# Optimization experiments

Hardware: AMD Instinct MI355X
Metric: run time of the kernel (lower is better)

## Reference

```python
import jax, jax.numpy as jnp
import numpy as np

_SAMPLING_EPS = 1e-5
_NEG_INF = -jnp.inf


def _apply_min_p(logits, min_p):
    # probs >= min_p * max_prob are kept (vLLM apply_min_p)
    probs = jax.nn.softmax(logits, axis=-1)
    max_p = jnp.max(probs, axis=-1, keepdims=True)
    keep = probs >= (min_p[:, None] * max_p)
    return jnp.where(keep, logits, _NEG_INF)


def _apply_top_k_top_p(logits, top_k, top_p):
    # One descending sort serves both filters (mirrors vLLM topk/topp kernel).
    T, V = logits.shape
    sorted_l = jnp.sort(logits, axis=-1)[:, ::-1]  # [T, V] descending
    # top-k threshold: k-th largest logit; top_k <= 0 means disabled
    k = jnp.where(top_k <= 0, V, jnp.clip(top_k, 1, V)).astype(jnp.int32)
    kth = jnp.take_along_axis(sorted_l, (k - 1)[:, None], axis=-1)  # [T, 1]
    # top-p: keep smallest prefix whose prob mass reaches top_p (first token always kept)
    probs = jax.nn.softmax(sorted_l, axis=-1)
    cum = jnp.cumsum(probs, axis=-1)
    keep_p = (cum - probs) < top_p[:, None]
    pth = jnp.min(jnp.where(keep_p, sorted_l, jnp.inf), axis=-1, keepdims=True)
    keep = (logits >= kth) & (logits >= pth)
    return jnp.where(keep, logits, _NEG_INF)


def _gather_logprobs(logprobs, num_logprobs, token_ids):
    # vLLM gather_logprobs: topk + sampled-token logprob + rank
    topk_lp, topk_idx = jax.lax.top_k(logprobs, num_logprobs)  # [T, K]
    tok = token_ids[:, None]  # [T, 1]
    tok_lp = jnp.take_along_axis(logprobs, tok, axis=-1)  # [T, 1]
    ranks = jnp.sum(logprobs >= tok_lp, axis=-1).astype(jnp.int32)  # [T]
    indices = jnp.concatenate([tok, topk_idx], axis=1).astype(jnp.int32)
    lps = jnp.concatenate([tok_lp, topk_lp], axis=1)
    return indices, lps, ranks


def setup_inputs() -> dict:
    key = jax.random.key(0)
    k1, k2, k3, k4, k5, k6 = jax.random.split(key, 6)
    T, V = 256, 128256
    logits = jax.random.normal(k1, (T, V), dtype=jnp.float32)
    temperature = 0.2 + 1.3 * jax.random.uniform(k2, (T,), dtype=jnp.float32)
    # every 8th request is greedy (temperature < _SAMPLING_EPS path)
    temperature = jnp.where(jnp.arange(T) % 8 == 0, 0.0, temperature)
    min_p = 0.05 * jax.random.uniform(k3, (T,), dtype=jnp.float32)
    top_p = 0.5 + 0.5 * jax.random.uniform(k4, (T,), dtype=jnp.float32)
    top_k = jax.random.randint(k5, (T,), 0, 64, dtype=jnp.int32)
    u = jax.random.uniform(k6, (T, V), dtype=jnp.float32, minval=1e-10, maxval=1.0)
    return {"logits": logits, "temperature": temperature, "min_p": min_p,
            "top_p": top_p, "top_k": top_k, "u": u, "num_logprobs": 20}


def reference(logits, temperature, min_p, top_p, top_k, u, num_logprobs):
    logits = logits.astype(jnp.float32)
    # logprobs computed on raw (pre-temperature) logits, as in vLLM
    raw_logprobs = jax.nn.log_softmax(logits, axis=-1)
    # greedy path
    greedy = jnp.argmax(logits, axis=-1)
    # random path: temperature -> min_p -> top-k/top-p -> gumbel-max sample
    is_greedy = temperature < _SAMPLING_EPS
    safe_temp = jnp.where(is_greedy, 1.0, temperature)  # rows with temp<eps use greedy anyway
    l = logits / safe_temp[:, None]
    l = _apply_min_p(l, min_p)
    l = _apply_top_k_top_p(l, top_k, top_p)
    gumbel = -jnp.log(-jnp.log(u))  # u in (0,1)
    random_sampled = jnp.argmax(l + gumbel, axis=-1)
    sampled = jnp.where(is_greedy, greedy, random_sampled)
    indices, lps, ranks = _gather_logprobs(raw_logprobs, num_logprobs, sampled)
    sampled_token_ids = sampled.astype(jnp.int32)[:, None]  # [T, 1]
    return sampled_token_ids, indices, lps, ranks
```

## Files before the change

kernel.cpp:

```cpp
#include <hip/hip_runtime.h>
#include <math.h>

#define TPB 1024
#define TPBS 256
#define NS 8
#define NBINS 512
#define CAP 2048
#define NSEL 64
#define MBINS 1024
#define MWIN 16.0f
#define WIN 2.0f
#define SLCAP 1024
#define BANDCAP 64

typedef unsigned long long u64t;

__device__ __forceinline__ unsigned int ordAsc(float v) {
  unsigned int b = __float_as_uint(v);
  return (b & 0x80000000u) ? ~b : (b | 0x80000000u);
}
__device__ __forceinline__ float ordInv(unsigned int o) {
  return __uint_as_float((o & 0x80000000u) ? (o & 0x7fffffffu) : ~o);
}
__device__ __forceinline__ unsigned int fkeyDesc(float v) { return ~ordAsc(v); }
// ... 41 lines not shown
  __syncthreads();
  return r;
}
__device__ __forceinline__ u64t blockMaxU64(u64t v, u64t* sred) {
  #pragma unroll
  for (int o = 32; o > 0; o >>= 1) { u64t v2 = __shfl_down(v, o, 64); if (v2 > v) v = v2; }
  int wid = threadIdx.x >> 6, lane = threadIdx.x & 63, nw = blockDim.x >> 6;
  __syncthreads();
  if (lane == 0) sred[wid] = v;
  __syncthreads();
  if (threadIdx.x == 0) { u64t r = sred[0]; for (int w = 1; w < nw; ++w) if (sred[w] > r) r = sred[w]; sred[0] = r; }
  __syncthreads();
  u64t r = sred[0];
  __syncthreads();
  return r;
}
__device__ __forceinline__ void blockArgMaxF(float& v, int& idx, float* sredf, int* sredi) {
  #pragma unroll
  for (int o = 32; o > 0; o >>= 1) {
    float v2 = __shfl_down(v, o, 64);
    int  i2 = __shfl_down(idx, o, 64);
    if (v2 > v || (v2 == v && i2 < idx)) { v = v2; idx = i2; }
  }
  int wid = threadIdx.x >> 6, lane = threadIdx.x & 63, nw = blockDim.x >> 6;
  __syncthreads();
  if (lane == 0) { sredf[wid] = v; sredi[wid] = idx; }
  __syncthreads();
  if (threadIdx.x == 0) {
    float bv = sredf[0]; int bi = sredi[0];
    for (int w = 1; w < nw; ++w) {
      float v2 = sredf[w]; int i2 = sredi[w];
      if (v2 > bv || (v2 == bv && i2 < bi)) { bv = v2; bi = i2; }
    }
    sredf[0] = bv; sredi[0] = bi;
  }
  __syncthreads();
  v = sredf[0]; idx = sredi[0];
  __syncthreads();
}

__device__ void bitonicSortN(u64t* keys, int n) {
  for (unsigned int k = 2; k <= (unsigned int)n; k <<= 1) {
    for (unsigned int j = k >> 1; j > 0; j >>= 1) {
      __syncthreads();
      for (unsigned int i = threadIdx.x; i < (unsigned int)n; i += blockDim.x) {
        unsigned int ixj = i ^ j;
        if (ixj > i) {
          u64t a = keys[i], b = keys[ixj];
          bool up = ((i & k) == 0);
          if ((a > b) == up) { keys[i] = b; keys[ixj] = a; }
        }
      }
    }
  }
  __syncthreads();
}

__device__ u64t bitonicReg1024(u64t key, u64t* lds) {
  const int tid = threadIdx.x;
  for (unsigned int k = 2; k <= 1024; k <<= 1) {
    for (unsigned int j = k >> 1; j > 0; j >>= 1) {
      u64t partner;
      if (j >= 64) {
        __syncthreads();
        lds[tid] = key;
        __syncthreads();
        partner = lds[tid ^ j];
      } else {
        partner = __shfl_xor((unsigned long long)key, (int)j, 64);
      }
      bool up = ((tid & k) == 0);
      bool lower = ((tid & j) == 0);
      bool keepSmaller = (up == lower);
      bool pSmaller = (partner < key);
      if (keepSmaller == pSmaller) key = partner;
    }
  }
  __syncthreads();
  lds[tid] = key;
  __syncthreads();
  return key;
}

__global__ __launch_bounds__(TPBS) void k1_max(const float* __restrict__ logits,
                                               u64t* __restrict__ maxes,
                                               int* __restrict__ ccnt,
                                               int* __restrict__ bandcnt,
                                               u64t* __restrict__ mass, int V) {
  const int row = blockIdx.y, s = blockIdx.x, tid = threadIdx.x;
  {
    const int per = MBINS / NS;
    u64t* m = mass + (size_t)row * MBINS + s * per;
    for (int b = tid; b < per; b += TPBS) m[b] = 0ull;
    if (s == 0 && tid == 0) { ccnt[row] = 0; bandcnt[row] = 0; }
  }
  const float* x = logits + (size_t)row * V;
  const int V4 = V >> 2;
  const float4* x4 = (const float4*)x;
  const int a4 = (int)(((long long)V4 * s) / NS), b4 = (int)(((long long)V4 * (s + 1)) / NS);
  u64t best = 0ull;
  for (int i4 = a4 + tid; i4 < b4; i4 += TPBS) {
    float4 v = x4[i4]; int b = i4 << 2;
    u64t k0 = mkMaxKey(v.x, b);     if (k0 > best) best = k0;
    u64t k1 = mkMaxKey(v.y, b + 1); if (k1 > best) best = k1;
    u64t k2 = mkMaxKey(v.z, b + 2); if (k2 > best) best = k2;
    u64t k3 = mkMaxKey(v.w, b + 3); if (k3 > best) best = k3;
  }
  if (s == NS - 1) for (int i = (V4 << 2) + tid; i < V; i += TPBS) {
    u64t k = mkMaxKey(x[i], i); if (k > best) best = k;
  }
  __shared__ u64t sred[16];
  best = blockMaxU64(best, sred);
  if (tid == 0) maxes[row * NS + s] = best;
}

__global__ __launch_bounds__(TPBS) void k2_all(const float* __restrict__ logits,
    const float* __restrict__ temp_arr, const float* __restrict__ minp_arr,
    const int* __restrict__ topk_arr, const u64t* __restrict__ maxes,
    float* __restrict__ s0_ws, float* __restrict__ sl_ws,
    float* __restrict__ sp_ws, int* __restrict__ ck_ws,
    int* __restrict__ ccnt, u64t* __restrict__ cand,
    int* __restrict__ bandcnt, u64t* __restrict__ band,
    u64t* __restrict__ mass, int V) {
  const int row = blockIdx.y, s = blockIdx.x, tid = threadIdx.x;
  __shared__ u64t smax[NS];
  __shared__ float sredF[16];
  __shared__ int sredI[16];
  __shared__ u64t lcand[SLCAP];
  __shared__ u64t lmass[MBINS];
  __shared__ int lcnt, lbase;
  const float temp = temp_arr[row];
  const bool greedy = (temp < 1e-5f);
  const int topk = topk_arr[row];
  const bool deep = (!greedy && topk <= 0);
  if (tid < NS) smax[tid] = maxes[row * NS + tid];
  if (tid == 0) lcnt = 0;
  if (deep) for (int b = tid; b < MBINS; b += TPBS) lmass[b] = 0ull;
  __syncthreads();
  u64t mk = smax[0];
  for (int w = 1; w < NS; ++w) { u64t t = smax[w]; if (t > mk) mk = t; }
  const float m0 = ordInv((unsigned int)(mk >> 32));
  const float st = greedy ? 1.0f : temp;
  const float ml = m0 / st;
  const float wlo = m0 - WIN;
  const float minp = minp_arr[row];
  const float bHi = minp * (1.0f + 4e-6f);
  const float bLo = minp * (1.0f - 4e-6f);
  const float scaleM = (float)MBINS / MWIN;
  const float* x = logits + (size_t)row * V;
  const int V4 = V >> 2;
  const float4* x4 = (const float4*)x;
  const int a4 = (int)(((long long)V4 * s) / NS), b4 = (int)(((long long)V4 * (s + 1)) / NS);
  float s0 = 0.f, sl = 0.f, sp = 0.f; int ckp = 0;
  auto body = [&](float vv, int gi) {
    s0 += expf(vv - m0);
    if (!greedy) {
      float l = vv / st;
      float e = expf(l - ml);
      sl += e;
      if (minp <= 0.f || e > bHi) {
        sp += e; ckp++;
        if (deep) {
          float fm = (m0 - vv) * scaleM;
          if (fm < (float)MBINS)
            atomicAdd(&lmass[(int)fm], (u64t)((double)e * 4294967296.0));
        }
      } else if (e >= bLo) {
        int pos = atomicAdd(&bandcnt[row], 1);
        if (pos < BANDCAP)
          band[(size_t)row * BANDCAP + pos] = ((u64t)(unsigned int)gi << 32) | __float_as_uint(vv);
      }
    }
    if (vv >= wlo) {
      int pos = atomicAdd(&lcnt, 1);
      if (pos < SLCAP) lcand[pos] = ((u64t)fkeyDesc(vv) << 32) | (unsigned int)gi;
    }
  };
  for (int i4 = a4 + tid; i4 < b4; i4 += TPBS) {
    float4 v = x4[i4]; int b = i4 << 2;
    body(v.x, b); body(v.y, b + 1); body(v.z, b + 2); body(v.w, b + 3);
  }
  if (s == NS - 1) for (int i = (V4 << 2) + tid; i < V; i += TPBS) body(x[i], i);
  float r0 = blockSumF(s0, sredF);
  float rl = blockSumF(sl, sredF);
  float rp = blockSumF(sp, sredF);
  int rc = blockSumI(ckp, sredI);
  if (tid == 0) {
    s0_ws[row * NS + s] = r0; sl_ws[row * NS + s] = rl;
    sp_ws[row * NS + s] = rp; ck_ws[row * NS + s] = rc;
    int c = lcnt;
    int add = (c > SLCAP) ? (c + CAP + 1) : c;
    lbase = atomicAdd(&ccnt[row], add);
  }
  __syncthreads();
  int c = lcnt < SLCAP ? lcnt : SLCAP;
  int base = lbase;
  for (int j = tid; j < c; j += TPBS) {
    int pos = base + j;
    if (pos < CAP) cand[(size_t)row * CAP + pos] = lcand[j];
  }
  if (deep) {
    for (int b = tid; b < MBINS; b += TPBS) {
      u64t m = lmass[b];
      if (m) atomicAdd(&mass[(size_t)row * MBINS + b], m);
    }
  }
}

__global__ __launch_bounds__(TPB) void k5_final(const float* __restrict__ logits,
    const float* __restrict__ temp_arr, const float* __restrict__ minp_arr,
    const float* __restrict__ topp_arr, const int* __restrict__ topk_arr,
    const float* __restrict__ u_arr, const u64t* __restrict__ maxes,
    const float* __restrict__ s0_ws, const float* __restrict__ sl_ws,
    const float* __restrict__ sp_ws, const int* __restrict__ ck_ws,
    int* __restrict__ ccnt, const u64t* __restrict__ cand,
    const u64t* __restrict__ mass, const u64t* __restrict__ band,
    const int* __restrict__ bandcnt, float* __restrict__ w_thr,
    int* __restrict__ w_bpM, double* __restrict__ w_seed, float* __restrict__ w_spD,
    float* __restrict__ out, int T, int V, int NL) {
  __shared__ u64t keyA[CAP];
  __shared__ u64t keyB[CAP];
  __shared__ int fh[NBINS];
  __shared__ float sredF[16];
  __shared__ int sredI[16];
  __shared__ u64t smax[NS];
  __shared__ float sp0[NS], spl[NS], spsp[NS];
  __shared__ int spck[NS];
  __shared__ float sh_thresh, sh_toklp, sh_spAdd;
  __shared__ double sh_seed;
  __shared__ int sh_cnt, sh_bp, sh_bCnt, sh_ckAdd;
  __shared__ u64t sh_bKeys[BANDCAP];
  __shared__ u64t sh_bMass[BANDCAP];
  __shared__ int  sh_bBin[BANDCAP];

  const int row = blockIdx.x;
  const int tid = threadIdx.x;
  const float* x  = logits + (size_t)row * V;
  const float* uu = u_arr  + (size_t)row * V;
  const float temp = temp_arr[row];
  const float minp = minp_arr[row];
  const float topp = topp_arr[row];
  const int   topk = topk_arr[row];
  const bool greedy = (temp < 1e-5f);
  const float st = greedy ? 1.0f : temp;
  const int V4 = V >> 2;
  const float4* x4 = (const float4*)x;

  if (tid < NS) {
    smax[tid] = maxes[row * NS + tid];
    sp0[tid] = s0_ws[row * NS + tid];
    spl[tid] = sl_ws[row * NS + tid];
    spsp[tid] = sp_ws[row * NS + tid];
    spck[tid] = ck_ws[row * NS + tid];
  }
  __syncthreads();
  u64t mk = smax[0];
  for (int w = 1; w < NS; ++w) { u64t t = smax[w]; if (t > mk) mk = t; }
  const float m0 = ordInv((unsigned int)(mk >> 32));
  const int gidx = (int)(~(unsigned int)mk);
  float S0 = sp0[0], S = spl[0], Sp = spsp[0];
  int ck = spck[0];
  for (int w = 1; w < NS; ++w) { S0 += sp0[w]; S += spl[w]; Sp += spsp[w]; ck += spck[w]; }
  const float ml = m0 / st;
  const float logS0 = logf(S0);
  const float rhs = minp * (1.0f / S);
  const float rhsS = rhs * S;
  const float rhsHi = rhsS * (1.0f + 1e-6f);
  const float rhsLo = rhsS * (1.0f - 1e-6f);
  auto keepTest = [&](float e) -> bool {
    if (e > rhsHi) return true;
    if (e < rhsLo) return false;
    return (e / S) >= rhs;
  };
  const bool deep = (!greedy && topk <= 0);
  const float scaleM = (float)MBINS / MWIN;

  const int bandTotal = greedy ? 0 : bandcnt[row];
  const bool bandOv = bandTotal > BANDCAP;
  if (tid == 0) { sh_bCnt = 0; sh_spAdd = 0.f; sh_ckAdd = 0; }
  __syncthreads();
  if (!greedy && !bandOv && bandTotal > 0 && minp > 0.f) {
    if (tid == 0) {
      for (int i = 0; i < bandTotal; ++i) sh_bKeys[i] = band[(size_t)row * BANDCAP + i];
      for (int i = 1; i < bandTotal; ++i) {
        u64t k = sh_bKeys[i]; int j = i - 1;
        while (j >= 0 && sh_bKeys[j] > k) { sh_bKeys[j + 1] = sh_bKeys[j]; j--; }
        sh_bKeys[j + 1] = k;
      }
      float spAdd = 0.f; int ckAdd = 0, bc = 0;
      for (int i = 0; i < bandTotal; ++i) {
        float vv = __uint_as_float((unsigned int)(sh_bKeys[i] & 0xffffffffu));
        float l = vv / st; float e = expf(l - ml);
        if ((e / S) >= rhs) {
          spAdd += e; ckAdd++;
          if (deep) {
            float fm = (m0 - vv) * scaleM;
            if (fm < (float)MBINS) { sh_bBin[bc] = (int)fm; sh_bMass[bc] = (u64t)((double)e * 4294967296.0); bc++; }
          }
        }
      }
      sh_spAdd = spAdd; sh_ckAdd = ckAdd; sh_bCnt = bc;
    }
    __syncthreads();
    Sp += sh_spAdd; ck += sh_ckAdd;
  } else if (!greedy && bandOv) {
    float sp2 = 0.f; int ck2 = 0;
    auto bodyR = [&](float vv) {
      float l = vv / st; float e = expf(l - ml);
      if (keepTest(e)) { sp2 += e; ck2++; }
    };
    for (int i4 = tid; i4 < V4; i4 += TPB) { float4 v = x4[i4]; bodyR(v.x); bodyR(v.y); bodyR(v.z); bodyR(v.w); }
    for (int i = (V4 << 2) + tid; i < V; i += TPB) bodyR(x[i]);
    Sp = blockSumF(sp2, sredF);
    ck = blockSumI(ck2, sredI);
  }

  int cc = ccnt[row];
  int Cact = cc < CAP ? cc : CAP;
  int need = NSEL;
  if (topk > need) need = topk;
  if (need > CAP / 2) need = CAP / 2;
  if (need > V) need = V;
  bool fb = (cc > CAP) || (Cact < need);
  if (!fb) {
    for (int j = tid; j < Cact; j += TPB) keyA[j] = cand[(size_t)row * CAP + j];
  } else {
    const float bS = (float)NBINS / MWIN;
    for (int b = tid; b < NBINS; b += TPB) fh[b] = 0;
    if (tid == 0) sh_cnt = 0;
    __syncthreads();
    auto hb = [&](float vv) {
      float fbv = (m0 - vv) * bS;
      if (fbv < (float)NBINS) atomicAdd(&fh[(int)fbv], 1);
    };
    for (int i4 = tid; i4 < V4; i4 += TPB) { float4 v = x4[i4]; hb(v.x); hb(v.y); hb(v.z); hb(v.w); }
    for (int i = (V4 << 2) + tid; i < V; i += TPB) hb(x[i]);
    __syncthreads();
    if (tid == 0) {
      int cum = 0, B = -1;
      for (int b = 0; b < NBINS; ++b) { cum += fh[b]; if (cum >= need) { B = b; break; } }
      if (B < 0) B = NBINS - 1;
      sh_bp = B;
    }
    __syncthreads();
    const int B = sh_bp;
    auto cb = [&](float vv, int gi) {
      float fbv = (m0 - vv) * bS;
      if (fbv < (float)NBINS && (int)fbv <= B) {
        int pos = atomicAdd(&sh_cnt, 1);
        if (pos < CAP) keyA[pos] = ((u64t)fkeyDesc(vv) << 32) | (unsigned int)gi;
      }
    };
    for (int i4 = tid; i4 < V4; i4 += TPB) { float4 v = x4[i4]; int b = i4 << 2; cb(v.x, b); cb(v.y, b + 1); cb(v.z, b + 2); cb(v.w, b + 3); }
    for (int i = (V4 << 2) + tid; i < V; i += TPB) cb(x[i], i);
    __syncthreads();
    Cact = sh_cnt < CAP ? sh_cnt : CAP;
  }
  __syncthreads();
  if (Cact <= 1024) {
    u64t ka = (tid < Cact) ? keyA[tid] : ~0ull;
    ka = bitonicReg1024(ka, keyA);
    u64t kb;
    if (tid < Cact) {
      float xv = fkeyInv((unsigned int)(ka >> 32));
      float lp = (xv - m0) - logS0;
      kb = ((u64t)fkeyDesc(lp) << 32) | (ka & 0xffffffffu);
    } else kb = ~0ull;
    bitonicReg1024(kb, keyB);
  } else {
    int n = 128; while (n < Cact) n <<= 1;
    for (int i = Cact + tid; i < n; i += TPB) keyA[i] = ~0ull;
    __syncthreads();
    bitonicSortN(keyA, n);
    for (int j = tid; j < n; j += TPB) {
      if (j < Cact) {
        u64t ka = keyA[j];
        float xv = fkeyInv((unsigned int)(ka >> 32));
        float lp = (xv - m0) - logS0;
        keyB[j] = ((u64t)fkeyDesc(lp) << 32) | (ka & 0xffffffffu);
      } else keyB[j] = ~0ull;
    }
    bitonicSortN(keyB, n);
  }

  int sampled = -1;
  if (greedy) {
    sampled = gidx;
  } else if (topk > 0) {
    if (tid == 0) {
      int k = topk; if (k > V) k = V; if (k > CAP) k = CAP;
      int jp = 0; float cum = 0.f;
      for (int j = 0; j < k; ++j) {
        float pj = 0.f;
        if (j < ck && j < Cact) {
          float xv = fkeyInv((unsigned int)(keyA[j] >> 32));
          pj = expf(xv / st - ml) / Sp;
        }
        cum += pj;
        float ex = cum - pj;
        if (ex < topp) jp = j;
      }
      float thr;
      if (jp < ck && jp < Cact) {
        float xv = fkeyInv((unsigned int)(keyA[jp] >> 32));
        thr = xv / st;
      } else thr = -INFINITY;
      sh_thresh = thr;
    }
    __syncthreads();
    const float thr = sh_thresh;
    float bm = -INFINITY; int bi = 0x7fffffff;
    for (int j = tid; j < Cact; j += TPB) {
      u64t ka = keyA[j];
      float xv = fkeyInv((unsigned int)(ka >> 32));
      int gi = (int)(ka & 0xffffffffu);
      float l = xv / st;
      float e = expf(l - ml);
      if (keepTest(e) && l >= thr) {
        float uv = uu[gi];
        float g = -logf(-logf(uv));
        float val = l + g;
        if (val > bm || (val == bm && gi < bi)) { bm = val; bi = gi; }
      }
    }
    blockArgMaxF(bm, bi, sredF, sredI);
    sampled = bi;
  } else {
    if (!bandOv) {
      if (tid < MBINS) {
        u64t m = mass[(size_t)row * MBINS + tid];
        int bc = sh_bCnt;
        for (int j = 0; j < bc; ++j) if (sh_bBin[j] == tid) m += sh_bMass[j];
        keyA[tid] = m;
      }
    } else {
      for (int b = tid; b < MBINS; b += TPB) keyA[b] = 0ull;
      __syncthreads();
      auto bodyM = [&](float vv) {
        float l = vv / st; float e = expf(l - ml);
        if (keepTest(e)) {
          float fm = (m0 - vv) * scaleM;
          if (fm < (float)MBINS) atomicAdd(&keyA[(int)fm], (u64t)((double)e * 4294967296.0));
        }
      };
      for (int i4 = tid; i4 < V4; i4 += TPB) { float4 v = x4[i4]; bodyM(v.x); bodyM(v.y); bodyM(v.z); bodyM(v.w); }
      for (int i = (V4 << 2) + tid; i < V; i += TPB) bodyM(x[i]);
    }
    __syncthreads();
    u64t mh = (tid < MBINS) ? keyA[tid] : 0ull;
    for (int off = 1; off < MBINS; off <<= 1) {
      u64t add = (tid < MBINS && tid >= off) ? keyA[tid - off] : 0ull;
      __syncthreads();
      if (tid < MBINS) keyA[tid] += add;
      __syncthreads();
    }
    const double TP = (double)topp * (double)Sp;
    int q = -1; u64t myexcl = 0;
    if (tid < MBINS && mh > 0ull) {
      u64t excl = keyA[tid] - mh;
      if ((double)excl * (1.0 / 4294967296.0) < TP) { q = tid; myexcl = excl; }
    }
    int bp = blockMaxI(q, sredI);
    if (bp >= 0 && tid == bp) sh_seed = (double)myexcl * (1.0 / 4294967296.0);
    if (bp < 0 && tid == 0) sh_seed = 0.0;
    __syncthreads();
    if (tid == 0) {
      w_bpM[row] = bp;
      w_seed[row] = sh_seed;
      w_spD[row] = Sp;
      ccnt[row] = 0;
      if (bp < 0) w_thr[row] = -INFINITY;
    }
  }

  if (!deep) {
    if (tid == 0) sh_toklp = (x[sampled] - m0) - logS0;
    __syncthreads();
    const float toklp = sh_toklp;
    int rc = 0;
    for (int j = tid; j < Cact; j += TPB) {
      float xv = fkeyInv((unsigned int)(keyA[j] >> 32));
      float lp = (xv - m0) - logS0;
      if (lp >= toklp) rc++;
    }
    int rank = blockSumI(rc, sredI);
    float* o_samp = out;
    float* o_idx  = out + T;
    float* o_lps  = out + T + (size_t)T * (NL + 1);
    float* o_rank = out + T + (size_t)2 * T * (NL + 1);
    if (tid == 0) {
      o_samp[row] = (float)sampled;
      o_idx[(size_t)row * (NL + 1)] = (float)sampled;
      o_lps[(size_t)row * (NL + 1)] = toklp;
      o_rank[row] = (float)rank;
    }
  }
  {
    float* o_idx  = out + T;
    float* o_lps  = out + T + (size_t)T * (NL + 1);
    for (int j = tid; j < NL; j += TPB) {
      u64t kb = keyB[j];
      o_idx[(size_t)row * (NL + 1) + 1 + j] = (float)(unsigned int)(kb & 0xffffffffu);
      o_lps[(size_t)row * (NL + 1) + 1 + j] = fkeyInv((unsigned int)(kb >> 32));
    }
  }
}

__global__ __launch_bounds__(TPBS) void k5b_collect(const float* __restrict__ logits,
    const float* __restrict__ temp_arr, const float* __restrict__ minp_arr,
    const int* __restrict__ topk_arr, const u64t* __restrict__ maxes,
    const float* __restrict__ sl_ws, const int* __restrict__ w_bpM,
    int* __restrict__ ccnt, u64t* __restrict__ cand, int V) {
  const int row = blockIdx.y, s = blockIdx.x, tid = threadIdx.x;
  const float temp = temp_arr[row];
  if (temp < 1e-5f || topk_arr[row] > 0) return;
  const int bp = w_bpM[row];
  if (bp < 0) return;
  __shared__ u64t smax[NS];
  __shared__ float ssl[NS];
  __shared__ u64t lcand[SLCAP];
  __shared__ int lcnt, lbase;
  if (tid < NS) { smax[tid] = maxes[row * NS + tid]; ssl[tid] = sl_ws[row * NS + tid]; }
  if (tid == 0) lcnt = 0;
  __syncthreads();
  u64t mk = smax[0];
  for (int w = 1; w < NS; ++w) { u64t t = smax[w]; if (t > mk) mk = t; }
  float S = ssl[0];
  for (int w = 1; w < NS; ++w) S += ssl[w];
  const float m0 = ordInv((unsigned int)(mk >> 32));
  const float st = temp;
  const float ml = m0 / st;
  const float minp = minp_arr[row];
  const float rhs = minp * (1.0f / S);
  const float rhsS = rhs * S;
  const float rhsHi = rhsS * (1.0f + 1e-6f);
  const float rhsLo = rhsS * (1.0f - 1e-6f);
  auto keepTest = [&](float e) -> bool {
    if (e > rhsHi) return true;
    if (e < rhsLo) return false;
    return (e / S) >= rhs;
  };
  const float scaleM = (float)MBINS / MWIN;
  const float* x = logits + (size_t)row * V;
  const int V4 = V >> 2;
  const float4* x4 = (const float4*)x;
  const int a4 = (int)(((long long)V4 * s) / NS), b4 = (int)(((long long)V4 * (s + 1)) / NS);
  auto body = [&](float vv, int gi) {
    float fm = (m0 - vv) * scaleM;
    if (fm < (float)MBINS && (int)fm == bp) {
      float l = vv / st;
      float e = expf(l - ml);
      if (keepTest(e)) {
        int pos = atomicAdd(&lcnt, 1);
        if (pos < SLCAP) lcand[pos] = ((u64t)fkeyDesc(vv) << 32) | (unsigned int)gi;
      }
    }
  };
  for (int i4 = a4 + tid; i4 < b4; i4 += TPBS) {
    float4 v = x4[i4]; int b = i4 << 2;
    body(v.x, b); body(v.y, b + 1); body(v.z, b + 2); body(v.w, b + 3);
  }
  if (s == NS - 1) for (int i = (V4 << 2) + tid; i < V; i += TPBS) body(x[i], i);
  __syncthreads();
  if (tid == 0) {
    int c = lcnt < SLCAP ? lcnt : SLCAP;
    lbase = atomicAdd(&ccnt[row], c);
  }
  __syncthreads();
  int c = lcnt < SLCAP ? lcnt : SLCAP;
  int base = lbase;
  for (int j = tid; j < c; j += TPBS) {
    int pos = base + j;
    if (pos < CAP) cand[(size_t)row * CAP + pos] = lcand[j];
  }
}

__global__ __launch_bounds__(TPB) void k5c_thr(const float* __restrict__ temp_arr,
    const float* __restrict__ topp_arr, const int* __restrict__ topk_arr,
    const u64t* __restrict__ maxes, const int* __restrict__ w_bpM,
    const int* __restrict__ ccnt, const u64t* __restrict__ cand,
    const float* __restrict__ w_spD, const double* __restrict__ w_seed,
    float* __restrict__ w_thr) {
  const int row = blockIdx.x, tid = threadIdx.x;
  const float temp = temp_arr[row];
  if (temp < 1e-5f || topk_arr[row] > 0) return;
  const int bp = w_bpM[row];
  if (bp < 0) return;
  __shared__ u64t keyA[CAP];
  __shared__ float pvals[CAP];
  __shared__ u64t smax[NS];
  if (tid < NS) smax[tid] = maxes[row * NS + tid];
  __syncthreads();
  u64t mk = smax[0];
  for (int w = 1; w < NS; ++w) { u64t t = smax[w]; if (t > mk) mk = t; }
  const float m0 = ordInv((unsigned int)(mk >> 32));
  const float st = temp;
  const float ml = m0 / st;
  const float Sp = w_spD[row];
  const double seed = w_seed[row];
  const float topp = topp_arr[row];
  int cc = ccnt[row];
  int C5 = cc < CAP ? cc : CAP;
  if (C5 <= 1024) {
    u64t kc = (tid < C5) ? cand[(size_t)row * CAP + tid] : ~0ull;
    bitonicReg1024(kc, keyA);
  } else {
    for (int j = tid; j < CAP; j += TPB)
      keyA[j] = (j < C5) ? cand[(size_t)row * CAP + j] : ~0ull;
    int n5 = 128; while (n5 < C5) n5 <<= 1;
    __syncthreads();
    bitonicSortN(keyA, n5);
  }
  for (int j = tid; j < C5; j += TPB) {
    float xv = fkeyInv((unsigned int)(keyA[j] >> 32));
    pvals[j] = expf(xv / st - ml) / Sp;
  }
  __syncthreads();
  if (tid == 0) {
    float cum = (float)(seed / (double)Sp);
    float lastVal = fkeyInv((unsigned int)(keyA[0] >> 32));
    for (int j = 0; j < C5; ++j) {
      float pj = pvals[j];
      cum += pj;
      float ex = cum - pj;
      if (ex < topp) lastVal = fkeyInv((unsigned int)(keyA[j] >> 32));
    }
    w_thr[row] = lastVal / st;
  }
}

__global__ __launch_bounds__(TPBS) void k6_gumbel(const float* __restrict__ logits,
    const float* __restrict__ temp_arr, const float* __restrict__ minp_arr,
    const int* __restrict__ topk_arr, const float* __restrict__ u_arr,
    const u64t* __restrict__ maxes, const float* __restrict__ sl_ws,
    const float* __restrict__ w_thr, u64t* __restrict__ gkey, int V) {
  const int row = blockIdx.y, s = blockIdx.x, tid = threadIdx.x;
  const float temp = temp_arr[row];
  if (temp < 1e-5f || topk_arr[row] > 0) return;
  __shared__ u64t smax[NS];
  __shared__ float ssl[NS];
  __shared__ float sredF[16];
  __shared__ int sredI[16];
  if (tid < NS) { smax[tid] = maxes[row * NS + tid]; ssl[tid] = sl_ws[row * NS + tid]; }
  __syncthreads();
  u64t mk = smax[0];
  for (int w = 1; w < NS; ++w) { u64t t = smax[w]; if (t > mk) mk = t; }
  float S = ssl[0];
  for (int w = 1; w < NS; ++w) S += ssl[w];
  const float m0 = ordInv((unsigned int)(mk >> 32));
  const float st = temp;
  const float ml = m0 / st;
  const float minp = minp_arr[row];
  const float rhs = minp * (1.0f / S);
  const float rhsS = rhs * S;
  const float rhsHi = rhsS * (1.0f + 1e-6f);
  const float rhsLo = rhsS * (1.0f - 1e-6f);
  auto keepTest = [&](float e) -> bool {
    if (e > rhsHi) return true;
    if (e < rhsLo) return false;
    return (e / S) >= rhs;
  };
  const float thr = w_thr[row];
  const float* x  = logits + (size_t)row * V;
  const float* uu = u_arr  + (size_t)row * V;
  const int V4 = V >> 2;
  const float4* x4 = (const float4*)x;
  const float4* u4 = (const float4*)uu;
  const int a4 = (int)(((long long)V4 * s) / NS), b4 = (int)(((long long)V4 * (s + 1)) / NS);
  float bm = -INFINITY; int bi = 0x7fffffff;
  auto body = [&](float vv, float uv, int gi) {
    float l = vv / st;
    float e = expf(l - ml);
    if (keepTest(e) && l >= thr) {
      float g = -logf(-logf(uv));
      float val = l + g;
      if (val > bm || (val == bm && gi < bi)) { bm = val; bi = gi; }
    }
  };
  for (int i4 = a4 + tid; i4 < b4; i4 += TPBS) {
    float4 v = x4[i4]; float4 w = u4[i4]; int b = i4 << 2;
    body(v.x, w.x, b); body(v.y, w.y, b + 1); body(v.z, w.z, b + 2); body(v.w, w.w, b + 3);
  }
  if (s == NS - 1) for (int i = (V4 << 2) + tid; i < V; i += TPBS) body(x[i], uu[i], i);
  blockArgMaxF(bm, bi, sredF, sredI);
  if (tid == 0) gkey[row * NS + s] = mkMaxKey(bm, bi);
}

__global__ __launch_bounds__(TPB) void k7_deepfin(const float* __restrict__ logits,
    const float* __restrict__ temp_arr, const int* __restrict__ topk_arr,
    const u64t* __restrict__ gkey, const float* __restrict__ s0_ws,
    const u64t* __restrict__ maxes, float* __restrict__ out, int T, int V, int NL) {
  const int row = blockIdx.x, tid = threadIdx.x;
  const float temp = temp_arr[row];
  if (temp < 1e-5f || topk_arr[row] > 0) return;
  __shared__ u64t sg[NS];
  __shared__ u64t smax[NS];
  __shared__ float sp0[NS];
  __shared__ int sredI[16];
  if (tid < NS) { sg[tid] = gkey[row * NS + tid]; smax[tid] = maxes[row * NS + tid]; sp0[tid] = s0_ws[row * NS + tid]; }
  __syncthreads();
  u64t gk = sg[0];
  for (int w = 1; w < NS; ++w) { if (sg[w] > gk) gk = sg[w]; }
  u64t mk = smax[0];
  for (int w = 1; w < NS; ++w) { u64t t = smax[w]; if (t > mk) mk = t; }
  float S0 = sp0[0];
  for (int w = 1; w < NS; ++w) S0 += sp0[w];
  const float m0 = ordInv((unsigned int)(mk >> 32));
  const float logS0 = logf(S0);
  const int sampled = (int)(~(unsigned int)gk);
  const float* x = logits + (size_t)row * V;
  const float toklp = (x[sampled] - m0) - logS0;
  const int V4 = V >> 2;
  const float4* x4 = (const float4*)x;
  int rc = 0;
  auto body = [&](float vv) {
    float lp = (vv - m0) - logS0;
    if (lp >= toklp) rc++;
  };
  for (int i4 = tid; i4 < V4; i4 += TPB) { float4 v = x4[i4]; body(v.x); body(v.y); body(v.z); body(v.w); }
  for (int i = (V4 << 2) + tid; i < V; i += TPB) body(x[i]);
  int rank = blockSumI(rc, sredI);
  float* o_samp = out;
  float* o_idx  = out + T;
  float* o_lps  = out + T + (size_t)T * (NL + 1);
  float* o_rank = out + T + (size_t)2 * T * (NL + 1);
  if (tid == 0) {
    o_samp[row] = (float)sampled;
    o_idx[(size_t)row * (NL + 1)] = (float)sampled;
    o_lps[(size_t)row * (NL + 1)] = toklp;
    o_rank[row] = (float)rank;
  }
}

__global__ __launch_bounds__(TPB) void sampler_mono(
    const float* __restrict__ logits, const float* __restrict__ temp_arr,
    const float* __restrict__ minp_arr, const float* __restrict__ topp_arr,
    const int* __restrict__ topk_arr, const float* __restrict__ u_arr,
    float* __restrict__ out, int T, int V, int NL) {
  __shared__ u64t keyA[CAP];
  __shared__ u64t keyB[CAP];
  __shared__ float pvals[CAP];
  __shared__ int   cnthist[NBINS];
  __shared__ u64t  masshist[NBINS];
  __shared__ float sredF[16];
  __shared__ int   sredI[16];
  __shared__ float sh_thresh, sh_toklp, sh_Rm, sh_Roff;
  __shared__ double sh_seedD, sh_seedBase;
  __shared__ int sh_B64, sh_Bp, sh_cnt, sh_state;

  const int row = blockIdx.x;
  const int tid = threadIdx.x;
  const float* x  = logits + (size_t)row * V;
  const float* uu = u_arr  + (size_t)row * V;
  const float temp = temp_arr[row];
  const float minp = minp_arr[row];
  const float topp = topp_arr[row];
  const int   topk = topk_arr[row];
  const bool greedy = (temp < 1e-5f);
  const float st = greedy ? 1.0f : temp;
  const int V4 = V >> 2;
  const float4* x4 = (const float4*)x;

  float m0; int gidx;
  {
    float lm = -INFINITY; int lidx = 0x7fffffff;
    for (int i4 = tid; i4 < V4; i4 += TPB) {
      float4 v = x4[i4]; int b = i4 << 2;
      if (v.x > lm) { lm = v.x; lidx = b; }
      if (v.y > lm) { lm = v.y; lidx = b + 1; }
      if (v.z > lm) { lm = v.z; lidx = b + 2; }
      if (v.w > lm) { lm = v.w; lidx = b + 3; }
    }
    for (int i = (V4 << 2) + tid; i < V; i += TPB) {
      float v = x[i]; if (v > lm) { lm = v; lidx = i; }
    }
    blockArgMaxF(lm, lidx, sredF, sredI);
    m0 = lm; gidx = lidx;
  }
  const float ml = m0 / st;

  float Rcur = 2.0f;
  float binScale = (float)NBINS / Rcur;
  for (int b = tid; b < NBINS; b += TPB) cnthist[b] = 0;
  __syncthreads();
  float S0, S;
  {
    float s0p = 0.f, slp = 0.f;
    auto histAdd = [&](float vv) {
      float fb = (m0 - vv) * binScale;
      if (fb < (float)NBINS) atomicAdd(&cnthist[(int)fb], 1);
// ... 250 lines not shown
      sh_thresh = lastVal / st;
    }
    __syncthreads();
    const float thr = sh_thresh;
    const float4* u4 = (const float4*)uu;
    float bm = -INFINITY; int bi = 0x7fffffff;
    auto body6 = [&](float vv, float uv, int gi) {
      float l = vv / st;
      float e = expf(l - ml);
      if (keepTest(e) && l >= thr) {
        float g = -logf(-logf(uv));
        float val = l + g;
        if (val > bm || (val == bm && gi < bi)) { bm = val; bi = gi; }
      }
    };
    for (int i4 = tid; i4 < V4; i4 += TPB) {
      float4 v = x4[i4]; float4 w = u4[i4]; int b = i4 << 2;
      body6(v.x, w.x, b); body6(v.y, w.y, b + 1); body6(v.z, w.z, b + 2); body6(v.w, w.w, b + 3);
    }
    for (int i = (V4 << 2) + tid; i < V; i += TPB) body6(x[i], uu[i], i);
    blockArgMaxF(bm, bi, sredF, sredI);
    sampled = bi;
  }

  if (tid == 0) sh_toklp = (x[sampled] - m0) - logS0;
  __syncthreads();
  const float toklp = sh_toklp;
  int rank;
  {
    int rc = 0;
    if (!needMass) {
      for (int j = tid; j < Cact; j += TPB) {
        float xv = fkeyInv((unsigned int)(keyA[j] >> 32));
        float lp = (xv - m0) - logS0;
        if (lp >= toklp) rc++;
      }
    } else {
      auto body7 = [&](float vv) {
        float lp = (vv - m0) - logS0;
        if (lp >= toklp) rc++;
      };
      for (int i4 = tid; i4 < V4; i4 += TPB) {
        float4 v = x4[i4]; body7(v.x); body7(v.y); body7(v.z); body7(v.w);
      }
      for (int i = (V4 << 2) + tid; i < V; i += TPB) body7(x[i]);
    }
    rank = blockSumI(rc, sredI);
  }

  float* o_samp = out;
  float* o_idx  = out + T;
  float* o_lps  = out + T + (size_t)T * (NL + 1);
  float* o_rank = out + T + (size_t)2 * T * (NL + 1);
  if (tid == 0) {
    o_samp[row] = (float)sampled;
    o_idx[(size_t)row * (NL + 1)] = (float)sampled;
    o_lps[(size_t)row * (NL + 1)] = toklp;
    o_rank[row] = (float)rank;
  }
  for (int j = tid; j < NL; j += TPB) {
    u64t kb = keyB[j];
    o_idx[(size_t)row * (NL + 1) + 1 + j] = (float)(unsigned int)(kb & 0xffffffffu);
    o_lps[(size_t)row * (NL + 1) + 1 + j] = fkeyInv((unsigned int)(kb >> 32));
  }
}

extern "C" void kernel_launch(void* const* d_in, const int* in_sizes, int n_in,
                              void* d_out, int out_size, void* d_ws, size_t ws_size,
                              hipStream_t stream) {
  const float* logits = (const float*)d_in[0];
  const float* temp   = (const float*)d_in[1];
  const float* minp   = (const float*)d_in[2];
  const float* topp   = (const float*)d_in[3];
  const int*   topk   = (const int*)d_in[4];
  const float* u      = (const float*)d_in[5];
  const int T  = in_sizes[1];
  const int V  = in_sizes[0] / T;
  const int NL = (out_size / T - 4) / 2;

  size_t off = 0;
  char* base = (char*)d_ws;
  u64t*   w_maxes   = (u64t*)(base + off);   off += (size_t)T * NS * 8;
  u64t*   w_cand    = (u64t*)(base + off);   off += (size_t)T * CAP * 8;
  u64t*   w_mass    = (u64t*)(base + off);   off += (size_t)T * MBINS * 8;
  u64t*   w_gkey    = (u64t*)(base + off);   off += (size_t)T * NS * 8;
  u64t*   w_band    = (u64t*)(base + off);   off += (size_t)T * BANDCAP * 8;
  double* w_seed    = (double*)(base + off); off += (size_t)T * 8;
  float*  w_s0      = (float*)(base + off);  off += (size_t)T * NS * 4;
  float*  w_sl      = (float*)(base + off);  off += (size_t)T * NS * 4;
  float*  w_sp      = (float*)(base + off);  off += (size_t)T * NS * 4;
  int*    w_ck      = (int*)(base + off);    off += (size_t)T * NS * 4;
  int*    w_ccnt    = (int*)(base + off);    off += (size_t)T * 4;
  int*    w_bandcnt = (int*)(base + off);    off += (size_t)T * 4;
  float*  w_thr     = (float*)(base + off);  off += (size_t)T * 4;
  int*    w_bpM     = (int*)(base + off);    off += (size_t)T * 4;
  float*  w_spD     = (float*)(base + off);  off += (size_t)T * 4;

  if (off > ws_size) {
    sampler_mono<<<T, TPB, 0, stream>>>(logits, temp, minp, topp, topk, u,
                                        (float*)d_out, T, V, NL);
    return;
  }

  dim3 gS(NS, T);
  k1_max<<<gS, TPBS, 0, stream>>>(logits, w_maxes, w_ccnt, w_bandcnt, w_mass, V);
  k2_all<<<gS, TPBS, 0, stream>>>(logits, temp, minp, topk, w_maxes, w_s0, w_sl,
                                  w_sp, w_ck, w_ccnt, w_cand, w_bandcnt, w_band,
                                  w_mass, V);
  k5_final<<<T, TPB, 0, stream>>>(logits, temp, minp, topp, topk, u, w_maxes,
                                  w_s0, w_sl, w_sp, w_ck, w_ccnt, w_cand, w_mass,
                                  w_band, w_bandcnt, w_thr, w_bpM, w_seed, w_spD,
                                  (float*)d_out, T, V, NL);
  k5b_collect<<<gS, TPBS, 0, stream>>>(logits, temp, minp, topk, w_maxes, w_sl,
                                       w_bpM, w_ccnt, w_cand, V);
  k5c_thr<<<T, TPB, 0, stream>>>(temp, topp, topk, w_maxes, w_bpM, w_ccnt, w_cand,
                                 w_spD, w_seed, w_thr);
  k6_gumbel<<<gS, TPBS, 0, stream>>>(logits, temp, minp, topk, u, w_maxes, w_sl,
                                     w_thr, w_gkey, V);
  k7_deepfin<<<T, TPB, 0, stream>>>(logits, temp, topk, w_gkey, w_s0, w_maxes,
                                    (float*)d_out, T, V, NL);
}
```

Measured before the change: 219.8 us.

## Move raw softmax sum into max pass, merge collect/threshold kernels, cut second sort

The raw-logit exp-sum now runs in the max kernel against the per-slice max and is merged later with exp(max_s - m0) rescaling. This lets greedy rows in k2 skip all exp work. Per-slice mass histograms are written without global atomics and no longer need zero-initialisation, at the cost of a summation over slices in k5. k5b_collect and k5c_thr are merged into one per-row kernel that rescans the row and sorts in shared memory, which drops a launch and the global candidate round trip. The second full bitonic sort of logprob keys is replaced by a rank sort over the top 64 candidates.

```diff
diff --git a/kernel.cpp b/kernel.cpp
--- a/kernel.cpp
+++ b/kernel.cpp
@@ -147,18 +147,22 @@
   return key;
 }
 
+__device__ __forceinline__ float combineS0(const u64t* smax, const float* s0s, float m0) {
+  float S0 = 0.f;
+  for (int w = 0; w < NS; ++w) {
+    float ms = ordInv((unsigned int)(smax[w] >> 32));
+    S0 += s0s[w] * expf(ms - m0);
+  }
+  return S0;
+}
+
 __global__ __launch_bounds__(TPBS) void k1_max(const float* __restrict__ logits,
                                                u64t* __restrict__ maxes,
+                                               float* __restrict__ s0_ws,
                                                int* __restrict__ ccnt,
-                                               int* __restrict__ bandcnt,
-                                               u64t* __restrict__ mass, int V) {
+                                               int* __restrict__ bandcnt, int V) {
   const int row = blockIdx.y, s = blockIdx.x, tid = threadIdx.x;
-  {
-    const int per = MBINS / NS;
-    u64t* m = mass + (size_t)row * MBINS + s * per;
-    for (int b = tid; b < per; b += TPBS) m[b] = 0ull;
-    if (s == 0 && tid == 0) { ccnt[row] = 0; bandcnt[row] = 0; }
-  }
+  if (s == 0 && tid == 0) { ccnt[row] = 0; bandcnt[row] = 0; }
   const float* x = logits + (size_t)row * V;
   const int V4 = V >> 2;
   const float4* x4 = (const float4*)x;
@@ -174,16 +178,25 @@
   if (s == NS - 1) for (int i = (V4 << 2) + tid; i < V; i += TPBS) {
     u64t k = mkMaxKey(x[i], i); if (k > best) best = k;
   }
-  __shared__ u64t sred[16];
-  best = blockMaxU64(best, sred);
+  __shared__ u64t sredU[16];
+  __shared__ float sredF[16];
+  best = blockMaxU64(best, sredU);
   if (tid == 0) maxes[row * NS + s] = best;
+  const float msv = ordInv((unsigned int)(best >> 32));
+  float s0 = 0.f;
+  for (int i4 = a4 + tid; i4 < b4; i4 += TPBS) {
+    float4 v = x4[i4];
+    s0 += expf(v.x - msv) + expf(v.y - msv) + expf(v.z - msv) + expf(v.w - msv);
+  }
+  if (s == NS - 1) for (int i = (V4 << 2) + tid; i < V; i += TPBS) s0 += expf(x[i] - msv);
+  float r0 = blockSumF(s0, sredF);
+  if (tid == 0) s0_ws[row * NS + s] = r0;
 }
 
 __global__ __launch_bounds__(TPBS) void k2_all(const float* __restrict__ logits,
     const float* __restrict__ temp_arr, const float* __restrict__ minp_arr,
     const int* __restrict__ topk_arr, const u64t* __restrict__ maxes,
-    float* __restrict__ s0_ws, float* __restrict__ sl_ws,
-    float* __restrict__ sp_ws, int* __restrict__ ck_ws,
+    float* __restrict__ sl_ws, float* __restrict__ sp_ws, int* __restrict__ ck_ws,
     int* __restrict__ ccnt, u64t* __restrict__ cand,
     int* __restrict__ bandcnt, u64t* __restrict__ band,
     u64t* __restrict__ mass, int V) {
@@ -205,36 +218,63 @@
   u64t mk = smax[0];
   for (int w = 1; w < NS; ++w) { u64t t = smax[w]; if (t > mk) mk = t; }
   const float m0 = ordInv((unsigned int)(mk >> 32));
-  const float st = greedy ? 1.0f : temp;
+  const float wlo = m0 - WIN;
+  const float* x = logits + (size_t)row * V;
+  const int V4 = V >> 2;
+  const float4* x4 = (const float4*)x;
+  const int a4 = (int)(((long long)V4 * s) / NS), b4 = (int)(((long long)V4 * (s + 1)) / NS);
+
+  if (greedy) {
+    auto bodyG = [&](float vv, int gi) {
+      if (vv >= wlo) {
+        int pos = atomicAdd(&lcnt, 1);
+        if (pos < SLCAP) lcand[pos] = ((u64t)fkeyDesc(vv) << 32) | (unsigned int)gi;
+      }
+    };
+    for (int i4 = a4 + tid; i4 < b4; i4 += TPBS) {
+      float4 v = x4[i4]; int b = i4 << 2;
+      bodyG(v.x, b); bodyG(v.y, b + 1); bodyG(v.z, b + 2); bodyG(v.w, b + 3);
+    }
+    if (s == NS - 1) for (int i = (V4 << 2) + tid; i < V; i += TPBS) bodyG(x[i], i);
+    __syncthreads();
+    if (tid == 0) {
+      sl_ws[row * NS + s] = 0.f; sp_ws[row * NS + s] = 0.f; ck_ws[row * NS + s] = 0;
+      int c = lcnt;
+      int add = (c > SLCAP) ? (c + CAP + 1) : c;
+      lbase = atomicAdd(&ccnt[row], add);
+    }
+    __syncthreads();
+    int c = lcnt < SLCAP ? lcnt : SLCAP;
+    int base = lbase;
+    for (int j = tid; j < c; j += TPBS) {
+      int pos = base + j;
+      if (pos < CAP) cand[(size_t)row * CAP + pos] = lcand[j];
+    }
+    return;
+  }
+
+  const float st = temp;
   const float ml = m0 / st;
-  const float wlo = m0 - WIN;
   const float minp = minp_arr[row];
   const float bHi = minp * (1.0f + 4e-6f);
   const float bLo = minp * (1.0f - 4e-6f);
   const float scaleM = (float)MBINS / MWIN;
-  const float* x = logits + (size_t)row * V;
-  const int V4 = V >> 2;
-  const float4* x4 = (const float4*)x;
-  const int a4 = (int)(((long long)V4 * s) / NS), b4 = (int)(((long long)V4 * (s + 1)) / NS);
-  float s0 = 0.f, sl = 0.f, sp = 0.f; int ckp = 0;
+  float sl = 0.f, sp = 0.f; int ckp = 0;
   auto body = [&](float vv, int gi) {
-    s0 += expf(vv - m0);
-    if (!greedy) {
-      float l = vv / st;
-      float e = expf(l - ml);
-      sl += e;
-      if (minp <= 0.f || e > bHi) {
-        sp += e; ckp++;
-        if (deep) {
-          float fm = (m0 - vv) * scaleM;
-          if (fm < (float)MBINS)
-            atomicAdd(&lmass[(int)fm], (u64t)((double)e * 4294967296.0));
-        }
-      } else if (e >= bLo) {
-        int pos = atomicAdd(&bandcnt[row], 1);
-        if (pos < BANDCAP)
-          band[(size_t)row * BANDCAP + pos] = ((u64t)(unsigned int)gi << 32) | __float_as_uint(vv);
-      }
+    float l = vv / st;
+    float e = expf(l - ml);
+    sl += e;
+    if (minp <= 0.f || e > bHi) {
+      sp += e; ckp++;
+      if (deep) {
+        float fm = (m0 - vv) * scaleM;
+        if (fm < (float)MBINS)
+          atomicAdd(&lmass[(int)fm], (u64t)((double)e * 4294967296.0));
+      }
+    } else if (e >= bLo) {
+      int pos = atomicAdd(&bandcnt[row], 1);
+      if (pos < BANDCAP)
+        band[(size_t)row * BANDCAP + pos] = ((u64t)(unsigned int)gi << 32) | __float_as_uint(vv);
     }
     if (vv >= wlo) {
       int pos = atomicAdd(&lcnt, 1);
@@ -246,13 +286,11 @@
     body(v.x, b); body(v.y, b + 1); body(v.z, b + 2); body(v.w, b + 3);
   }
   if (s == NS - 1) for (int i = (V4 << 2) + tid; i < V; i += TPBS) body(x[i], i);
-  float r0 = blockSumF(s0, sredF);
   float rl = blockSumF(sl, sredF);
   float rp = blockSumF(sp, sredF);
   int rc = blockSumI(ckp, sredI);
   if (tid == 0) {
-    s0_ws[row * NS + s] = r0; sl_ws[row * NS + s] = rl;
-    sp_ws[row * NS + s] = rp; ck_ws[row * NS + s] = rc;
+    sl_ws[row * NS + s] = rl; sp_ws[row * NS + s] = rp; ck_ws[row * NS + s] = rc;
     int c = lcnt;
     int add = (c > SLCAP) ? (c + CAP + 1) : c;
     lbase = atomicAdd(&ccnt[row], add);
@@ -265,10 +303,8 @@
     if (pos < CAP) cand[(size_t)row * CAP + pos] = lcand[j];
   }
   if (deep) {
-    for (int b = tid; b < MBINS; b += TPBS) {
-      u64t m = lmass[b];
-      if (m) atomicAdd(&mass[(size_t)row * MBINS + b], m);
-    }
+    u64t* mrow = mass + ((size_t)row * NS + s) * MBINS;
+    for (int b = tid; b < MBINS; b += TPBS) mrow[b] = lmass[b];
   }
 }
 
@@ -278,13 +314,12 @@
     const float* __restrict__ u_arr, const u64t* __restrict__ maxes,
     const float* __restrict__ s0_ws, const float* __restrict__ sl_ws,
     const float* __restrict__ sp_ws, const int* __restrict__ ck_ws,
-    int* __restrict__ ccnt, const u64t* __restrict__ cand,
+    const int* __restrict__ ccnt, const u64t* __restrict__ cand,
     const u64t* __restrict__ mass, const u64t* __restrict__ band,
     const int* __restrict__ bandcnt, float* __restrict__ w_thr,
     int* __restrict__ w_bpM, double* __restrict__ w_seed, float* __restrict__ w_spD,
     float* __restrict__ out, int T, int V, int NL) {
   __shared__ u64t keyA[CAP];
-  __shared__ u64t keyB[CAP];
   __shared__ int fh[NBINS];
   __shared__ float sredF[16];
   __shared__ int sredI[16];
@@ -297,6 +332,8 @@
   __shared__ u64t sh_bKeys[BANDCAP];
   __shared__ u64t sh_bMass[BANDCAP];
   __shared__ int  sh_bBin[BANDCAP];
+  __shared__ u64t kb64[NSEL];
+  __shared__ u64t kbs[NSEL];
 
   const int row = blockIdx.x;
   const int tid = threadIdx.x;
@@ -323,9 +360,10 @@
   for (int w = 1; w < NS; ++w) { u64t t = smax[w]; if (t > mk) mk = t; }
   const float m0 = ordInv((unsigned int)(mk >> 32));
   const int gidx = (int)(~(unsigned int)mk);
-  float S0 = sp0[0], S = spl[0], Sp = spsp[0];
+  float S = spl[0], Sp = spsp[0];
   int ck = spck[0];
-  for (int w = 1; w < NS; ++w) { S0 += sp0[w]; S += spl[w]; Sp += spsp[w]; ck += spck[w]; }
+  for (int w = 1; w < NS; ++w) { S += spl[w]; Sp += spsp[w]; ck += spck[w]; }
+  const float S0 = combineS0(smax, sp0, m0);
   const float ml = m0 / st;
   const float logS0 = logf(S0);
   const float rhs = minp * (1.0f / S);
@@ -424,28 +462,38 @@
   __syncthreads();
   if (Cact <= 1024) {
     u64t ka = (tid < Cact) ? keyA[tid] : ~0ull;
-    ka = bitonicReg1024(ka, keyA);
-    u64t kb;
-    if (tid < Cact) {
-      float xv = fkeyInv((unsigned int)(ka >> 32));
-      float lp = (xv - m0) - logS0;
-      kb = ((u64t)fkeyDesc(lp) << 32) | (ka & 0xffffffffu);
-    } else kb = ~0ull;
-    bitonicReg1024(kb, keyB);
+    bitonicReg1024(ka, keyA);
   } else {
     int n = 128; while (n < Cact) n <<= 1;
     for (int i = Cact + tid; i < n; i += TPB) keyA[i] = ~0ull;
     __syncthreads();
     bitonicSortN(keyA, n);
-    for (int j = tid; j < n; j += TPB) {
-      if (j < Cact) {
-        u64t ka = keyA[j];
-        float xv = fkeyInv((unsigned int)(ka >> 32));
-        float lp = (xv - m0) - logS0;
-        keyB[j] = ((u64t)fkeyDesc(lp) << 32) | (ka & 0xffffffffu);
-      } else keyB[j] = ~0ull;
-    }
-    bitonicSortN(keyB, n);
+  }
+  {
+    int M = Cact < NSEL ? Cact : NSEL;
+    if (tid < M) {
+      u64t ka = keyA[tid];
+      float xv = fkeyInv((unsigned int)(ka >> 32));
+      float lp = (xv - m0) - logS0;
+      kb64[tid] = ((u64t)fkeyDesc(lp) << 32) | (ka & 0xffffffffu);
+    }
+    __syncthreads();
+    if (tid < M) {
+      u64t me = kb64[tid];
+      int r = 0;
+      for (int i = 0; i < M; ++i) r += (kb64[i] < me) ? 1 : 0;
+      kbs[r] = me;
+    }
+    __syncthreads();
+    float* o_idx  = out + T;
+    float* o_lps  = out + T + (size_t)T * (NL + 1);
+    for (int j = tid; j < NL; j += TPB) {
+      if (j < M) {
+        u64t kb = kbs[j];
+        o_idx[(size_t)row * (NL + 1) + 1 + j] = (float)(unsigned int)(kb & 0xffffffffu);
+        o_lps[(size_t)row * (NL + 1) + 1 + j] = fkeyInv((unsigned int)(kb >> 32));
+      }
+    }
   }
 
   int sampled = -1;
@@ -493,7 +541,8 @@
   } else {
     if (!bandOv) {
       if (tid < MBINS) {
-        u64t m = mass[(size_t)row * MBINS + tid];
+        u64t m = 0;
+        for (int w = 0; w < NS; ++w) m += mass[((size_t)row * NS + w) * MBINS + tid];
         int bc = sh_bCnt;
         for (int j = 0; j < bc; ++j) if (sh_bBin[j] == tid) m += sh_bMass[j];
         keyA[tid] = m;
@@ -533,7 +582,6 @@
       w_bpM[row] = bp;
       w_seed[row] = sh_seed;
       w_spD[row] = Sp;
-      ccnt[row] = 0;
       if (bp < 0) w_thr[row] = -INFINITY;
     }
   }
@@ -560,33 +608,26 @@
       o_rank[row] = (float)rank;
     }
   }
-  {
-    float* o_idx  = out + T;
-    float* o_lps  = out + T + (size_t)T * (NL + 1);
-    for (int j = tid; j < NL; j += TPB) {
-      u64t kb = keyB[j];
-      o_idx[(size_t)row * (NL + 1) + 1 + j] = (float)(unsigned int)(kb & 0xffffffffu);
-      o_lps[(size_t)row * (NL + 1) + 1 + j] = fkeyInv((unsigned int)(kb >> 32));
-    }
-  }
-}
-
-__global__ __launch_bounds__(TPBS) void k5b_collect(const float* __restrict__ logits,
+}
+
+__global__ __launch_bounds__(TPB) void kD_thr(const float* __restrict__ logits,
     const float* __restrict__ temp_arr, const float* __restrict__ minp_arr,
-    const int* __restrict__ topk_arr, const u64t* __restrict__ maxes,
-    const float* __restrict__ sl_ws, const int* __restrict__ w_bpM,
-    int* __restrict__ ccnt, u64t* __restrict__ cand, int V) {
-  const int row = blockIdx.y, s = blockIdx.x, tid = threadIdx.x;
+    const float* __restrict__ topp_arr, const int* __restrict__ topk_arr,
+    const u64t* __restrict__ maxes, const float* __restrict__ sl_ws,
+    const int* __restrict__ w_bpM, const float* __restrict__ w_spD,
+    const double* __restrict__ w_seed, float* __restrict__ w_thr, int V) {
+  const int row = blockIdx.x, tid = threadIdx.x;
   const float temp = temp_arr[row];
   if (temp < 1e-5f || topk_arr[row] > 0) return;
   const int bp = w_bpM[row];
   if (bp < 0) return;
+  __shared__ u64t keyA[CAP];
+  __shared__ float pvals[CAP];
   __shared__ u64t smax[NS];
   __shared__ float ssl[NS];
-  __shared__ u64t lcand[SLCAP];
-  __shared__ int lcnt, lbase;
+  __shared__ int sh_cnt;
   if (tid < NS) { smax[tid] = maxes[row * NS + tid]; ssl[tid] = sl_ws[row * NS + tid]; }
-  if (tid == 0) lcnt = 0;
+  if (tid == 0) sh_cnt = 0;
   __syncthreads();
   u64t mk = smax[0];
   for (int w = 1; w < NS; ++w) { u64t t = smax[w]; if (t > mk) mk = t; }
@@ -609,80 +650,42 @@
   const float* x = logits + (size_t)row * V;
   const int V4 = V >> 2;
   const float4* x4 = (const float4*)x;
-  const int a4 = (int)(((long long)V4 * s) / NS), b4 = (int)(((long long)V4 * (s + 1)) / NS);
   auto body = [&](float vv, int gi) {
     float fm = (m0 - vv) * scaleM;
     if (fm < (float)MBINS && (int)fm == bp) {
       float l = vv / st;
       float e = expf(l - ml);
       if (keepTest(e)) {
-        int pos = atomicAdd(&lcnt, 1);
-        if (pos < SLCAP) lcand[pos] = ((u64t)fkeyDesc(vv) << 32) | (unsigned int)gi;
+        int pos = atomicAdd(&sh_cnt, 1);
+        if (pos < CAP) keyA[pos] = ((u64t)fkeyDesc(vv) << 32) | (unsigned int)gi;
       }
     }
   };
-  for (int i4 = a4 + tid; i4 < b4; i4 += TPBS) {
+  for (int i4 = tid; i4 < V4; i4 += TPB) {
     float4 v = x4[i4]; int b = i4 << 2;
     body(v.x, b); body(v.y, b + 1); body(v.z, b + 2); body(v.w, b + 3);
   }
-  if (s == NS - 1) for (int i = (V4 << 2) + tid; i < V; i += TPBS) body(x[i], i);
-  __syncthreads();
-  if (tid == 0) {
-    int c = lcnt < SLCAP ? lcnt : SLCAP;
-    lbase = atomicAdd(&ccnt[row], c);
-  }
-  __syncthreads();
-  int c = lcnt < SLCAP ? lcnt : SLCAP;
-  int base = lbase;
-  for (int j = tid; j < c; j += TPBS) {
-    int pos = base + j;
-    if (pos < CAP) cand[(size_t)row * CAP + pos] = lcand[j];
-  }
-}
-
-__global__ __launch_bounds__(TPB) void k5c_thr(const float* __restrict__ temp_arr,
-    const float* __restrict__ topp_arr, const int* __restrict__ topk_arr,
-    const u64t* __restrict__ maxes, const int* __restrict__ w_bpM,
-    const int* __restrict__ ccnt, const u64t* __restrict__ cand,
-    const float* __restrict__ w_spD, const double* __restrict__ w_seed,
-    float* __restrict__ w_thr) {
-  const int row = blockIdx.x, tid = threadIdx.x;
-  const float temp = temp_arr[row];
-  if (temp < 1e-5f || topk_arr[row] > 0) return;
-  const int bp = w_bpM[row];
-  if (bp < 0) return;
-  __shared__ u64t keyA[CAP];
-  __shared__ float pvals[CAP];
-  __shared__ u64t smax[NS];
-  if (tid < NS) smax[tid] = maxes[row * NS + tid];
-  __syncthreads();
-  u64t mk = smax[0];
-  for (int w = 1; w < NS; ++w) { u64t t = smax[w]; if (t > mk) mk = t; }
-  const float m0 = ordInv((unsigned int)(mk >> 32));
-  const float st = temp;
-  const float ml = m0 / st;
-  const float Sp = w_spD[row];
-  const double seed = w_seed[row];
-  const float topp = topp_arr[row];
-  int cc = ccnt[row];
-  int C5 = cc < CAP ? cc : CAP;
+  for (int i = (V4 << 2) + tid; i < V; i += TPB) body(x[i], i);
+  __syncthreads();
+  int C5 = sh_cnt < CAP ? sh_cnt : CAP;
   if (C5 <= 1024) {
-    u64t kc = (tid < C5) ? cand[(size_t)row * CAP + tid] : ~0ull;
+    u64t kc = (tid < C5) ? keyA[tid] : ~0ull;
     bitonicReg1024(kc, keyA);
   } else {
-    for (int j = tid; j < CAP; j += TPB)
-      keyA[j] = (j < C5) ? cand[(size_t)row * CAP + j] : ~0ull;
     int n5 = 128; while (n5 < C5) n5 <<= 1;
+    for (int i = C5 + tid; i < n5; i += TPB) keyA[i] = ~0ull;
     __syncthreads();
     bitonicSortN(keyA, n5);
   }
+  const float Sp = w_spD[row];
   for (int j = tid; j < C5; j += TPB) {
     float xv = fkeyInv((unsigned int)(keyA[j] >> 32));
     pvals[j] = expf(xv / st - ml) / Sp;
   }
   __syncthreads();
   if (tid == 0) {
-    float cum = (float)(seed / (double)Sp);
+    const float topp = topp_arr[row];
+    float cum = (float)(w_seed[row] / (double)Sp);
     float lastVal = fkeyInv((unsigned int)(keyA[0] >> 32));
     for (int j = 0; j < C5; ++j) {
       float pj = pvals[j];
@@ -768,9 +771,8 @@
   for (int w = 1; w < NS; ++w) { if (sg[w] > gk) gk = sg[w]; }
   u64t mk = smax[0];
   for (int w = 1; w < NS; ++w) { u64t t = smax[w]; if (t > mk) mk = t; }
-  float S0 = sp0[0];
-  for (int w = 1; w < NS; ++w) S0 += sp0[w];
   const float m0 = ordInv((unsigned int)(mk >> 32));
+  const float S0 = combineS0(smax, sp0, m0);
   const float logS0 = logf(S0);
   const int sampled = (int)(~(unsigned int)gk);
   const float* x = logits + (size_t)row * V;
@@ -1187,7 +1189,7 @@
   char* base = (char*)d_ws;
   u64t*   w_maxes   = (u64t*)(base + off);   off += (size_t)T * NS * 8;
   u64t*   w_cand    = (u64t*)(base + off);   off += (size_t)T * CAP * 8;
-  u64t*   w_mass    = (u64t*)(base + off);   off += (size_t)T * MBINS * 8;
+  u64t*   w_mass    = (u64t*)(base + off);   off += (size_t)T * NS * MBINS * 8;
   u64t*   w_gkey    = (u64t*)(base + off);   off += (size_t)T * NS * 8;
   u64t*   w_band    = (u64t*)(base + off);   off += (size_t)T * BANDCAP * 8;
   double* w_seed    = (double*)(base + off); off += (size_t)T * 8;
@@ -1208,18 +1210,16 @@
   }
 
   dim3 gS(NS, T);
-  k1_max<<<gS, TPBS, 0, stream>>>(logits, w_maxes, w_ccnt, w_bandcnt, w_mass, V);
-  k2_all<<<gS, TPBS, 0, stream>>>(logits, temp, minp, topk, w_maxes, w_s0, w_sl,
+  k1_max<<<gS, TPBS, 0, stream>>>(logits, w_maxes, w_s0, w_ccnt, w_bandcnt, V);
+  k2_all<<<gS, TPBS, 0, stream>>>(logits, temp, minp, topk, w_maxes, w_sl,
                                   w_sp, w_ck, w_ccnt, w_cand, w_bandcnt, w_band,
                                   w_mass, V);
   k5_final<<<T, TPB, 0, stream>>>(logits, temp, minp, topp, topk, u, w_maxes,
                                   w_s0, w_sl, w_sp, w_ck, w_ccnt, w_cand, w_mass,
                                   w_band, w_bandcnt, w_thr, w_bpM, w_seed, w_spD,
                                   (float*)d_out, T, V, NL);
-  k5b_collect<<<gS, TPBS, 0, stream>>>(logits, temp, minp, topk, w_maxes, w_sl,
-                                       w_bpM, w_ccnt, w_cand, V);
-  k5c_thr<<<T, TPB, 0, stream>>>(temp, topp, topk, w_maxes, w_bpM, w_ccnt, w_cand,
-                                 w_spD, w_seed, w_thr);
+  kD_thr<<<T, TPB, 0, stream>>>(logits, temp, minp, topp, topk, w_maxes, w_sl,
+                                w_bpM, w_spD, w_seed, w_thr, V);
   k6_gumbel<<<gS, TPBS, 0, stream>>>(logits, temp, minp, topk, u, w_maxes, w_sl,
                                      w_thr, w_gkey, V);
   k7_deepfin<<<T, TPB, 0, stream>>>(logits, temp, topk, w_gkey, w_s0, w_maxes,
```

Result: faster. 212.7 us (-3.2%).
